# Kernel tuning notes

Measured on AMD Instinct MI355X. Metric: run time of the kernel, lower is better.

## Reference

```python
import jax, jax.numpy as jnp
import numpy as np
import math

B, W, D_IN, H = 64, 512, 300, 512

def setup_inputs() -> dict:
    key = jax.random.key(0)
    ks = jax.random.split(key, 8)
    s = 1.0 / math.sqrt(D_IN)
    return {
        "char_vectors": jax.random.normal(ks[0], (B, W, D_IN), jnp.float32),
        "word_vectors": jax.random.normal(ks[1], (B, W, D_IN), jnp.float32),
        "Wk": jax.random.uniform(ks[2], (D_IN, H), jnp.float32, -s, s),
        "bk": jnp.zeros((H,), jnp.float32),
        "Wq": jax.random.uniform(ks[3], (D_IN, H), jnp.float32, -s, s),
        "bq": jnp.zeros((H,), jnp.float32),
        "Wv": jax.random.uniform(ks[4], (D_IN, H), jnp.float32, -s, s),
        "bv": jnp.zeros((H,), jnp.float32),
    }

def reference(char_vectors, word_vectors, Wk, bk, Wq, bq, Wv, bv):
    # Stack word/char reps per word -> [B, W, 2, H]
    def proj(Wm, bm):
        return jnp.stack([word_vectors @ Wm + bm, char_vectors @ Wm + bm], axis=2)
    K = proj(Wk, bk)
    Q = proj(Wq, bq)
    V = proj(Wv, bv)
    temp = jnp.sqrt(jnp.asarray(H, jnp.float32))
    # tiny 2x2 attention per word, fully batched (dropout off = eval mode)
    attn = jnp.einsum("bwqh,bwkh->bwqk", Q, K) / temp
    attn = jax.nn.softmax(attn, axis=-1)
    out = jnp.einsum("bwqk,bwkh->bwqh", attn, V)  # [B, W, 2, H]
    return out.reshape(B, W, 2 * H)
```

## Files before the change

kernel.cpp:

```cpp
#include <hip/hip_runtime.h>

#define D 300
#define HDIM 512
#define ROWS 128
#define WPB 64
#define KSTEPS 10
#define NCH 24
#define CH_BYTES 40960
#define CH_ELEMS 20480
#define SEGW 5

typedef __attribute__((ext_vector_type(4))) float f32x4;
typedef __attribute__((ext_vector_type(8))) short bf16x8;

__device__ inline unsigned short f2bf(float f) {
  unsigned int u = __float_as_uint(f);
  unsigned int r = (u + 0x7fffu + ((u >> 16) & 1u)) >> 16;
  return (unsigned short)r;
}

__device__ inline void gload_lds16(const void* g, void* l) {
  __builtin_amdgcn_global_load_lds(
      (const __attribute__((address_space(1))) unsigned int*)g,
      (__attribute__((address_space(3))) unsigned int*)l, 16, 0, 0);
}

__global__ __launch_bounds__(512) void prep_weights(
    const float* __restrict__ Wq, const float* __restrict__ Wk,
    const float* __restrict__ Wv, unsigned short* __restrict__ wt) {
  int idx = blockIdx.x * 512 + threadIdx.x;
  int c = idx / CH_ELEMS, r = idx - c * CH_ELEMS;
  int ks = r >> 11, r2 = r & 2047;
  int col = r2 >> 5, kk = r2 & 31;
  int k = ks * 32 + kk;
  const float* M; int gcol;
  if (c < 16) {
    if (col < 32) { M = Wq; gcol = c * 32 + col; }
    else          { M = Wk; gcol = c * 32 + col - 32; }
  } else { M = Wv; gcol = (c - 16) * 64 + col; }
  float v = (k < D) ? M[k * HDIM + gcol] : 0.0f;
  wt[idx] = f2bf(v);
}

__global__ __launch_bounds__(512) void fused_attn(
    const float* __restrict__ charv, const float* __restrict__ wordv,
    const unsigned short* __restrict__ wt,
    const float* __restrict__ bk, const float* __restrict__ bq,
    const float* __restrict__ bv, float* __restrict__ out) {
  extern __shared__ char lds[];
  float* biasL = (float*)(lds + 3 * CH_BYTES);
  float* sS    = biasL + 1536;
  float* sAt   = sS;

  const int tid  = threadIdx.x;
  const int wid  = tid >> 6;
  const int lane = tid & 63;
  const int lrow = lane & 15;
  const int kgrp = lane >> 4;
  const int rg   = wid >> 1;
  const int cg   = wid & 1;

  auto stage = [&](int t) {
    const char* src = (const char*)wt + (long)t * CH_BYTES + wid * (SEGW * 1024) + lane * 16;
    char* dst = lds + (t % 3) * CH_BYTES + wid * (SEGW * 1024);
#pragma unroll
    for (int j = 0; j < SEGW; ++j)
      gload_lds16(src + j * 1024, dst + j * 1024);
  };

  for (int i = tid; i < 1536; i += 512) {
    float v = (i < 512) ? bq[i] : ((i < 1024) ? bk[i - 512] : bv[i - 1024]);
    biasL[i] = v;
  }
  bf16x8 a[2][KSTEPS];
#pragma unroll
  for (int rt = 0; rt < 2; ++rt) {
    int row = blockIdx.x * ROWS + rg * 32 + rt * 16 + lrow;
    const float* rp = ((row & 1) ? charv : wordv) + (row >> 1) * D;
#pragma unroll
    for (int ks = 0; ks < KSTEPS; ++ks) {
      int k0 = ks * 32 + kgrp * 8;
      float4 lo = {0.f, 0.f, 0.f, 0.f}, hi = {0.f, 0.f, 0.f, 0.f};
      if (k0 + 8 <= D) {
        lo = *(const float4*)(rp + k0);
        hi = *(const float4*)(rp + k0 + 4);
      } else if (k0 < D) {
        lo = *(const float4*)(rp + k0);
      }
      bf16x8 v;
      v[0] = (short)f2bf(lo.x); v[1] = (short)f2bf(lo.y);
      v[2] = (short)f2bf(lo.z); v[3] = (short)f2bf(lo.w);
      v[4] = (short)f2bf(hi.x); v[5] = (short)f2bf(hi.y);
      v[6] = (short)f2bf(hi.z); v[7] = (short)f2bf(hi.w);
      a[rt][ks] = v;
    }
  }
  stage(0);
  stage(1);

  float p[2][8];
#pragma unroll
  for (int rt = 0; rt < 2; ++rt)
#pragma unroll
    for (int t = 0; t < 8; ++t) p[rt][t] = 0.f;

  const int fq = (cg * 16 + lrow) * 64 + kgrp * 16;

  for (int t = 0; t < 16; ++t) {
    asm volatile("s_waitcnt vmcnt(5)" ::: "memory");
    asm volatile("s_waitcnt lgkmcnt(0)" ::: "memory");
    __builtin_amdgcn_s_barrier();
    stage(t + 2);
    const char* buf = lds + (t % 3) * CH_BYTES;
    float bqv = biasL[t * 32 + cg * 16 + lrow];
    float bkv = biasL[512 + t * 32 + cg * 16 + lrow];
    f32x4 accQ[2], accK[2];
    accQ[0] = (f32x4){bqv, bqv, bqv, bqv}; accQ[1] = accQ[0];
    accK[0] = (f32x4){bkv, bkv, bkv, bkv}; accK[1] = accK[0];
#pragma unroll
    for (int ks = 0; ks < KSTEPS; ++ks) {
      bf16x8 bquf = *(const bf16x8*)(buf + ks * 4096 + fq);
      bf16x8 bkuf = *(const bf16x8*)(buf + ks * 4096 + fq + 2048);
      accQ[0] = __builtin_amdgcn_mfma_f32_16x16x32_bf16(a[0][ks], bquf, accQ[0], 0, 0, 0);
      accQ[1] = __builtin_amdgcn_mfma_f32_16x16x32_bf16(a[1][ks], bquf, accQ[1], 0, 0, 0);
      accK[0] = __builtin_amdgcn_mfma_f32_16x16x32_bf16(a[0][ks], bkuf, accK[0], 0, 0, 0);
      accK[1] = __builtin_amdgcn_mfma_f32_16x16x32_bf16(a[1][ks], bkuf, accK[1], 0, 0, 0);
    }
#pragma unroll
    for (int rt = 0; rt < 2; ++rt)
#pragma unroll
      for (int wl = 0; wl < 2; ++wl)
#pragma unroll
        for (int i = 0; i < 2; ++i)
#pragma unroll
          for (int j = 0; j < 2; ++j)
            p[rt][wl * 4 + i * 2 + j] += accQ[rt][wl * 2 + i] * accK[rt][wl * 2 + j];
  }

#pragma unroll
  for (int rt = 0; rt < 2; ++rt)
#pragma unroll
    for (int t = 0; t < 8; ++t) {
      float v = p[rt][t];
      v += __shfl_xor(v, 1);
      v += __shfl_xor(v, 2);
      v += __shfl_xor(v, 4);
      v += __shfl_xor(v, 8);
      p[rt][t] = v;
    }
  if (lrow == 0) {
#pragma unroll
    for (int rt = 0; rt < 2; ++rt)
#pragma unroll
      for (int t = 0; t < 8; ++t) {
        int w = rg * 16 + rt * 8 + kgrp * 2 + (t >> 2);
        sS[cg * 256 + w * 4 + (t & 3)] = p[rt][t];
      }
  }
  asm volatile("s_waitcnt lgkmcnt(0)" ::: "memory");
  __builtin_amdgcn_s_barrier();
  if (tid < 64) {
    const float sc = 0.044194173824159216f;
    float s[4];
#pragma unroll
    for (int t = 0; t < 4; ++t) s[t] = (sS[tid * 4 + t] + sS[256 + tid * 4 + t]) * sc;
#pragma unroll
    for (int i = 0; i < 2; ++i) {
      float m  = fmaxf(s[i * 2], s[i * 2 + 1]);
      float e0 = expf(s[i * 2] - m), e1 = expf(s[i * 2 + 1] - m);
      float inv = 1.0f / (e0 + e1);
      sAt[tid * 4 + i * 2]     = e0 * inv;
      sAt[tid * 4 + i * 2 + 1] = e1 * inv;
    }
  }
  asm volatile("s_waitcnt lgkmcnt(0)" ::: "memory");
  __builtin_amdgcn_s_barrier();

  float at0[2][4], at1[2][4];
#pragma unroll
  for (int rt = 0; rt < 2; ++rt) {
    int wA = rg * 16 + rt * 8 + kgrp * 2;
#pragma unroll
    for (int t = 0; t < 4; ++t) {
      at0[rt][t] = sAt[wA * 4 + t];
      at1[rt][t] = sAt[(wA + 1) * 4 + t];
    }
  }

  for (int t = 16; t < NCH; ++t) {
    if (t == 16) asm volatile("s_waitcnt vmcnt(5)" ::: "memory");
    else         asm volatile("s_waitcnt vmcnt(21)" ::: "memory");
    asm volatile("s_waitcnt lgkmcnt(0)" ::: "memory");
    __builtin_amdgcn_s_barrier();
    if (t + 2 < NCH) stage(t + 2);
    const char* buf = lds + (t % 3) * CH_BYTES;
    const int g = t - 16;
    f32x4 accV[2][2];
#pragma unroll
    for (int ct = 0; ct < 2; ++ct) {
      float b = biasL[1024 + g * 64 + cg * 32 + ct * 16 + lrow];
      accV[0][ct] = (f32x4){b, b, b, b};
      accV[1][ct] = accV[0][ct];
    }
    const int fv = (cg * 32 + lrow) * 64 + kgrp * 16;
#pragma unroll
    for (int ks = 0; ks < KSTEPS; ++ks) {
      bf16x8 b0 = *(const bf16x8*)(buf + ks * 4096 + fv);
      bf16x8 b1 = *(const bf16x8*)(buf + ks * 4096 + fv + 1024);
      accV[0][0] = __builtin_amdgcn_mfma_f32_16x16x32_bf16(a[0][ks], b0, accV[0][0], 0, 0, 0);
      accV[1][0] = __builtin_amdgcn_mfma_f32_16x16x32_bf16(a[1][ks], b0, accV[1][0], 0, 0, 0);
      accV[0][1] = __builtin_amdgcn_mfma_f32_16x16x32_bf16(a[0][ks], b1, accV[0][1], 0, 0, 0);
      accV[1][1] = __builtin_amdgcn_mfma_f32_16x16x32_bf16(a[1][ks], b1, accV[1][1], 0, 0, 0);
    }
#pragma unroll
    for (int rt = 0; rt < 2; ++rt) {
      int gA = blockIdx.x * WPB + rg * 16 + rt * 8 + kgrp * 2;
#pragma unroll
      for (int ct = 0; ct < 2; ++ct) {
        int h = g * 64 + cg * 32 + ct * 16 + lrow;
        float* o = out + gA * 1024 + h;
        o[0]    = at0[rt][0] * accV[rt][ct][0] + at0[rt][1] * accV[rt][ct][1];
        o[512]  = at0[rt][2] * accV[rt][ct][0] + at0[rt][3] * accV[rt][ct][1];
        o[1024] = at1[rt][0] * accV[rt][ct][2] + at1[rt][1] * accV[rt][ct][3];
        o[1536] = at1[rt][2] * accV[rt][ct][2] + at1[rt][3] * accV[rt][ct][3];
      }
    }
  }
}

extern "C" void kernel_launch(void* const* d_in, const int* in_sizes, int n_in,
                              void* d_out, int out_size, void* d_ws, size_t ws_size,
                              hipStream_t stream) {
  const float* charv = (const float*)d_in[0];
  const float* wordv = (const float*)d_in[1];
  const float* Wk = (const float*)d_in[2];
  const float* bk = (const float*)d_in[3];
  const float* Wq = (const float*)d_in[4];
  const float* bq = (const float*)d_in[5];
  const float* Wv = (const float*)d_in[6];
  const float* bv = (const float*)d_in[7];
  float* out = (float*)d_out;
  unsigned short* wt = (unsigned short*)d_ws;

  prep_weights<<<NCH * CH_ELEMS / 512, 512, 0, stream>>>(Wq, Wk, Wv, wt);

  const int lds_bytes = 3 * CH_BYTES + 1536 * 4 + 512 * 4;
  fused_attn<<<65536 / ROWS, 512, lds_bytes, stream>>>(charv, wordv, wt, bk, bq, bv, out);
}
```

Measured before the change: 98.64 us.

## Switch to 32x32x16 MFMA with 256-row blocks and reorganized weight layout

Replaces the 16x16x32 bf16 MFMA tiles with 32x32x16 tiles, so each wave owns 32 rows across all 32 columns of a chunk. Block size doubles from 128 to 256 rows, which halves the number of weight-chunk streams per row and removes the cross-wave score reduction. The weight prep kernel now writes a new K-interleaved layout that matches the larger MFMA operand shape. The cost is more registers per wave (f32x16 accumulators, 20 A fragments), fewer blocks in the grid, and a retuned vmcnt wait.

Result: faster. 87.47 us (-11.3%).

```diff
diff --git a/kernel.cpp b/kernel.cpp
--- a/kernel.cpp
+++ b/kernel.cpp
@@ -2,14 +2,16 @@
 
 #define D 300
 #define HDIM 512
-#define ROWS 128
-#define WPB 64
-#define KSTEPS 10
+#define ROWS 256
+#define WPB 128
+#define NKS 20
 #define NCH 24
 #define CH_BYTES 40960
 #define CH_ELEMS 20480
+#define REG_BYTES 20480
 #define SEGW 5
 
+typedef __attribute__((ext_vector_type(16))) float f32x16;
 typedef __attribute__((ext_vector_type(4))) float f32x4;
 typedef __attribute__((ext_vector_type(8))) short bf16x8;
 
@@ -29,15 +31,16 @@
     const float* __restrict__ Wq, const float* __restrict__ Wk,
     const float* __restrict__ Wv, unsigned short* __restrict__ wt) {
   int idx = blockIdx.x * 512 + threadIdx.x;
+  if (idx >= NCH * CH_ELEMS) return;
   int c = idx / CH_ELEMS, r = idx - c * CH_ELEMS;
-  int ks = r >> 11, r2 = r & 2047;
-  int col = r2 >> 5, kk = r2 & 31;
-  int k = ks * 32 + kk;
+  int reg = r / 10240, r2 = r - reg * 10240;
+  int ks = r2 >> 9, r3 = r2 & 511;
+  int kh = r3 >> 8, r4 = r3 & 255;
+  int col = r4 >> 3, e = r4 & 7;
+  int k = ks * 16 + kh * 8 + e;
   const float* M; int gcol;
-  if (c < 16) {
-    if (col < 32) { M = Wq; gcol = c * 32 + col; }
-    else          { M = Wk; gcol = c * 32 + col - 32; }
-  } else { M = Wv; gcol = (c - 16) * 64 + col; }
+  if (c < 16) { M = reg ? Wk : Wq; gcol = c * 32 + col; }
+  else        { M = Wv; gcol = (c - 16) * 64 + reg * 32 + col; }
   float v = (k < D) ? M[k * HDIM + gcol] : 0.0f;
   wt[idx] = f2bf(v);
 }
@@ -55,10 +58,8 @@
   const int tid  = threadIdx.x;
   const int wid  = tid >> 6;
   const int lane = tid & 63;
-  const int lrow = lane & 15;
-  const int kgrp = lane >> 4;
-  const int rg   = wid >> 1;
-  const int cg   = wid & 1;
+  const int lo5  = lane & 31;
+  const int hi   = lane >> 5;
 
   auto stage = [&](int t) {
     const char* src = (const char*)wt + (long)t * CH_BYTES + wid * (SEGW * 1024) + lane * 16;
@@ -72,98 +73,87 @@
     float v = (i < 512) ? bq[i] : ((i < 1024) ? bk[i - 512] : bv[i - 1024]);
     biasL[i] = v;
   }
-  bf16x8 a[2][KSTEPS];
-#pragma unroll
-  for (int rt = 0; rt < 2; ++rt) {
-    int row = blockIdx.x * ROWS + rg * 32 + rt * 16 + lrow;
+  bf16x8 a[NKS];
+  {
+    int row = blockIdx.x * ROWS + wid * 32 + lo5;
     const float* rp = ((row & 1) ? charv : wordv) + (row >> 1) * D;
 #pragma unroll
-    for (int ks = 0; ks < KSTEPS; ++ks) {
-      int k0 = ks * 32 + kgrp * 8;
-      float4 lo = {0.f, 0.f, 0.f, 0.f}, hi = {0.f, 0.f, 0.f, 0.f};
+    for (int ks = 0; ks < NKS; ++ks) {
+      int k0 = ks * 16 + hi * 8;
+      float4 lo = {0.f, 0.f, 0.f, 0.f}, hif = {0.f, 0.f, 0.f, 0.f};
       if (k0 + 8 <= D) {
-        lo = *(const float4*)(rp + k0);
-        hi = *(const float4*)(rp + k0 + 4);
+        lo  = *(const float4*)(rp + k0);
+        hif = *(const float4*)(rp + k0 + 4);
       } else if (k0 < D) {
-        lo = *(const float4*)(rp + k0);
+        lo  = *(const float4*)(rp + k0);
       }
       bf16x8 v;
-      v[0] = (short)f2bf(lo.x); v[1] = (short)f2bf(lo.y);
-      v[2] = (short)f2bf(lo.z); v[3] = (short)f2bf(lo.w);
-      v[4] = (short)f2bf(hi.x); v[5] = (short)f2bf(hi.y);
-      v[6] = (short)f2bf(hi.z); v[7] = (short)f2bf(hi.w);
-      a[rt][ks] = v;
+      v[0] = (short)f2bf(lo.x);  v[1] = (short)f2bf(lo.y);
+      v[2] = (short)f2bf(lo.z);  v[3] = (short)f2bf(lo.w);
+      v[4] = (short)f2bf(hif.x); v[5] = (short)f2bf(hif.y);
+      v[6] = (short)f2bf(hif.z); v[7] = (short)f2bf(hif.w);
+      a[ks] = v;
     }
   }
   stage(0);
   stage(1);
 
-  float p[2][8];
-#pragma unroll
-  for (int rt = 0; rt < 2; ++rt)
-#pragma unroll
-    for (int t = 0; t < 8; ++t) p[rt][t] = 0.f;
-
-  const int fq = (cg * 16 + lrow) * 64 + kgrp * 16;
+  float p[32];
+#pragma unroll
+  for (int t = 0; t < 32; ++t) p[t] = 0.f;
 
   for (int t = 0; t < 16; ++t) {
     asm volatile("s_waitcnt vmcnt(5)" ::: "memory");
     asm volatile("s_waitcnt lgkmcnt(0)" ::: "memory");
     __builtin_amdgcn_s_barrier();
     stage(t + 2);
-    const char* buf = lds + (t % 3) * CH_BYTES;
-    float bqv = biasL[t * 32 + cg * 16 + lrow];
-    float bkv = biasL[512 + t * 32 + cg * 16 + lrow];
-    f32x4 accQ[2], accK[2];
-    accQ[0] = (f32x4){bqv, bqv, bqv, bqv}; accQ[1] = accQ[0];
-    accK[0] = (f32x4){bkv, bkv, bkv, bkv}; accK[1] = accK[0];
-#pragma unroll
-    for (int ks = 0; ks < KSTEPS; ++ks) {
-      bf16x8 bquf = *(const bf16x8*)(buf + ks * 4096 + fq);
-      bf16x8 bkuf = *(const bf16x8*)(buf + ks * 4096 + fq + 2048);
-      accQ[0] = __builtin_amdgcn_mfma_f32_16x16x32_bf16(a[0][ks], bquf, accQ[0], 0, 0, 0);
-      accQ[1] = __builtin_amdgcn_mfma_f32_16x16x32_bf16(a[1][ks], bquf, accQ[1], 0, 0, 0);
-      accK[0] = __builtin_amdgcn_mfma_f32_16x16x32_bf16(a[0][ks], bkuf, accK[0], 0, 0, 0);
-      accK[1] = __builtin_amdgcn_mfma_f32_16x16x32_bf16(a[1][ks], bkuf, accK[1], 0, 0, 0);
-    }
-#pragma unroll
-    for (int rt = 0; rt < 2; ++rt)
-#pragma unroll
-      for (int wl = 0; wl < 2; ++wl)
-#pragma unroll
-        for (int i = 0; i < 2; ++i)
-#pragma unroll
-          for (int j = 0; j < 2; ++j)
-            p[rt][wl * 4 + i * 2 + j] += accQ[rt][wl * 2 + i] * accK[rt][wl * 2 + j];
-  }
-
-#pragma unroll
-  for (int rt = 0; rt < 2; ++rt)
-#pragma unroll
-    for (int t = 0; t < 8; ++t) {
-      float v = p[rt][t];
-      v += __shfl_xor(v, 1);
-      v += __shfl_xor(v, 2);
-      v += __shfl_xor(v, 4);
-      v += __shfl_xor(v, 8);
-      p[rt][t] = v;
-    }
-  if (lrow == 0) {
-#pragma unroll
-    for (int rt = 0; rt < 2; ++rt)
-#pragma unroll
-      for (int t = 0; t < 8; ++t) {
-        int w = rg * 16 + rt * 8 + kgrp * 2 + (t >> 2);
-        sS[cg * 256 + w * 4 + (t & 3)] = p[rt][t];
-      }
+    const char* base = lds + (t % 3) * CH_BYTES + hi * 512 + lo5 * 16;
+    float bqv = biasL[t * 32 + lo5];
+    float bkv = biasL[512 + t * 32 + lo5];
+    f32x16 accQ, accK;
+#pragma unroll
+    for (int r = 0; r < 16; ++r) { accQ[r] = bqv; accK[r] = bkv; }
+#pragma unroll
+    for (int ks = 0; ks < NKS; ++ks) {
+      bf16x8 qb = *(const bf16x8*)(base + ks * 1024);
+      bf16x8 kb = *(const bf16x8*)(base + REG_BYTES + ks * 1024);
+      accQ = __builtin_amdgcn_mfma_f32_32x32x16_bf16(a[ks], qb, accQ, 0, 0, 0);
+      accK = __builtin_amdgcn_mfma_f32_32x32x16_bf16(a[ks], kb, accK, 0, 0, 0);
+    }
+#pragma unroll
+    for (int tt = 0; tt < 8; ++tt)
+#pragma unroll
+      for (int i = 0; i < 2; ++i)
+#pragma unroll
+        for (int j = 0; j < 2; ++j)
+          p[tt * 4 + i * 2 + j] += accQ[2 * tt + i] * accK[2 * tt + j];
+  }
+
+#pragma unroll
+  for (int t = 0; t < 32; ++t) {
+    float v = p[t];
+    v += __shfl_xor(v, 1);
+    v += __shfl_xor(v, 2);
+    v += __shfl_xor(v, 4);
+    v += __shfl_xor(v, 8);
+    v += __shfl_xor(v, 16);
+    p[t] = v;
+  }
+  if (lo5 == 0) {
+#pragma unroll
+    for (int tt = 0; tt < 8; ++tt) {
+      int w = wid * 16 + (tt >> 1) * 4 + (tt & 1) + hi * 2;
+#pragma unroll
+      for (int q = 0; q < 4; ++q) sS[w * 4 + q] = p[tt * 4 + q];
+    }
   }
   asm volatile("s_waitcnt lgkmcnt(0)" ::: "memory");
   __builtin_amdgcn_s_barrier();
-  if (tid < 64) {
+  if (tid < 128) {
     const float sc = 0.044194173824159216f;
     float s[4];
 #pragma unroll
-    for (int t = 0; t < 4; ++t) s[t] = (sS[tid * 4 + t] + sS[256 + tid * 4 + t]) * sc;
+    for (int t = 0; t < 4; ++t) s[t] = sS[tid * 4 + t] * sc;
 #pragma unroll
     for (int i = 0; i < 2; ++i) {
       float m  = fmaxf(s[i * 2], s[i * 2 + 1]);
@@ -176,53 +166,40 @@
   asm volatile("s_waitcnt lgkmcnt(0)" ::: "memory");
   __builtin_amdgcn_s_barrier();
 
-  float at0[2][4], at1[2][4];
-#pragma unroll
-  for (int rt = 0; rt < 2; ++rt) {
-    int wA = rg * 16 + rt * 8 + kgrp * 2;
-#pragma unroll
-    for (int t = 0; t < 4; ++t) {
-      at0[rt][t] = sAt[wA * 4 + t];
-      at1[rt][t] = sAt[(wA + 1) * 4 + t];
-    }
+  f32x4 at[8];
+#pragma unroll
+  for (int tt = 0; tt < 8; ++tt) {
+    int w = wid * 16 + (tt >> 1) * 4 + (tt & 1) + hi * 2;
+    at[tt] = *(const f32x4*)(sAt + w * 4);
   }
 
   for (int t = 16; t < NCH; ++t) {
     if (t == 16) asm volatile("s_waitcnt vmcnt(5)" ::: "memory");
-    else         asm volatile("s_waitcnt vmcnt(21)" ::: "memory");
+    else         asm volatile("s_waitcnt vmcnt(37)" ::: "memory");
     asm volatile("s_waitcnt lgkmcnt(0)" ::: "memory");
     __builtin_amdgcn_s_barrier();
     if (t + 2 < NCH) stage(t + 2);
-    const char* buf = lds + (t % 3) * CH_BYTES;
+    const char* base = lds + (t % 3) * CH_BYTES + hi * 512 + lo5 * 16;
     const int g = t - 16;
-    f32x4 accV[2][2];
 #pragma unroll
     for (int ct = 0; ct < 2; ++ct) {
-      float b = biasL[1024 + g * 64 + cg * 32 + ct * 16 + lrow];
-      accV[0][ct] = (f32x4){b, b, b, b};
-      accV[1][ct] = accV[0][ct];
-    }
-    const int fv = (cg * 32 + lrow) * 64 + kgrp * 16;
-#pragma unroll
-    for (int ks = 0; ks < KSTEPS; ++ks) {
-      bf16x8 b0 = *(const bf16x8*)(buf + ks * 4096 + fv);
-      bf16x8 b1 = *(const bf16x8*)(buf + ks * 4096 + fv + 1024);
-      accV[0][0] = __builtin_amdgcn_mfma_f32_16x16x32_bf16(a[0][ks], b0, accV[0][0], 0, 0, 0);
-      accV[1][0] = __builtin_amdgcn_mfma_f32_16x16x32_bf16(a[1][ks], b0, accV[1][0], 0, 0, 0);
-      accV[0][1] = __builtin_amdgcn_mfma_f32_16x16x32_bf16(a[0][ks], b1, accV[0][1], 0, 0, 0);
-      accV[1][1] = __builtin_amdgcn_mfma_f32_16x16x32_bf16(a[1][ks], b1, accV[1][1], 0, 0, 0);
-    }
-#pragma unroll
-    for (int rt = 0; rt < 2; ++rt) {
-      int gA = blockIdx.x * WPB + rg * 16 + rt * 8 + kgrp * 2;
-#pragma unroll
-      for (int ct = 0; ct < 2; ++ct) {
-        int h = g * 64 + cg * 32 + ct * 16 + lrow;
-        float* o = out + gA * 1024 + h;
-        o[0]    = at0[rt][0] * accV[rt][ct][0] + at0[rt][1] * accV[rt][ct][1];
-        o[512]  = at0[rt][2] * accV[rt][ct][0] + at0[rt][3] * accV[rt][ct][1];
-        o[1024] = at1[rt][0] * accV[rt][ct][2] + at1[rt][1] * accV[rt][ct][3];
-        o[1536] = at1[rt][2] * accV[rt][ct][2] + at1[rt][3] * accV[rt][ct][3];
+      float bvv = biasL[1024 + g * 64 + ct * 32 + lo5];
+      f32x16 accV;
+#pragma unroll
+      for (int r = 0; r < 16; ++r) accV[r] = bvv;
+#pragma unroll
+      for (int ks = 0; ks < NKS; ++ks) {
+        bf16x8 vb = *(const bf16x8*)(base + ct * REG_BYTES + ks * 1024);
+        accV = __builtin_amdgcn_mfma_f32_32x32x16_bf16(a[ks], vb, accV, 0, 0, 0);
+      }
+      int h = g * 64 + ct * 32 + lo5;
+#pragma unroll
+      for (int tt = 0; tt < 8; ++tt) {
+        int w = wid * 16 + (tt >> 1) * 4 + (tt & 1) + hi * 2;
+        long gw = (long)(blockIdx.x * WPB + w);
+        float v0 = accV[2 * tt], v1 = accV[2 * tt + 1];
+        out[gw * 1024 + h]       = at[tt][0] * v0 + at[tt][1] * v1;
+        out[gw * 1024 + 512 + h] = at[tt][2] * v0 + at[tt][3] * v1;
       }
     }
   }
@@ -242,7 +219,7 @@
   float* out = (float*)d_out;
   unsigned short* wt = (unsigned short*)d_ws;
 
-  prep_weights<<<NCH * CH_ELEMS / 512, 512, 0, stream>>>(Wq, Wk, Wv, wt);
+  prep_weights<<<(NCH * CH_ELEMS + 511) / 512, 512, 0, stream>>>(Wq, Wk, Wv, wt);
 
   const int lds_bytes = 3 * CH_BYTES + 1536 * 4 + 512 * 4;
   fused_attn<<<65536 / ROWS, 512, lds_bytes, stream>>>(charv, wordv, wt, bk, bq, bv, out);
```
